# Optimization experiments

Hardware: AMD Instinct MI355X
Metric: run time of the kernel (lower is better)

Reference implementation:

```python
import jax, jax.numpy as jnp
import numpy as np

N = 100000   # nodes
E = 640000   # edges
DIN = 128
H = 128
DOUT = 64
EPS = 1e-5   # BatchNorm eps


def setup_inputs() -> dict:
    key = jax.random.key(0)
    ks = jax.random.split(key, 20)
    x = jax.random.normal(ks[0], (N, DIN), jnp.float32)
    edge_index = jax.random.randint(ks[1], (2, E), 0, N, dtype=jnp.int64)
    ricci_curvature = jax.random.normal(ks[2], (E,), jnp.float32)
    s = 0.05
    W1 = jax.random.normal(ks[3], (DIN, H), jnp.float32) * s
    b1 = jnp.zeros((H,), jnp.float32)
    Wm = jax.random.normal(ks[4], (H, H), jnp.float32) * s
    bm = jnp.zeros((H,), jnp.float32)
    W2 = jax.random.normal(ks[5], (H, DOUT), jnp.float32) * s
    b2 = jnp.zeros((DOUT,), jnp.float32)
    def bn_params(k, d):
        k1, k2, k3, k4 = jax.random.split(k, 4)
        g = jax.random.uniform(k1, (d,), jnp.float32) + 0.5
        b = jax.random.normal(k2, (d,), jnp.float32) * 0.1
        m = jax.random.normal(k3, (d,), jnp.float32) * 0.1
        v = jax.random.uniform(k4, (d,), jnp.float32) + 0.5
        return g, b, m, v
    bn1_g, bn1_b, bn1_m, bn1_v = bn_params(ks[6], DIN)
    bnm_g, bnm_b, bnm_m, bnm_v = bn_params(ks[7], H)
    bn2_g, bn2_b, bn2_m, bn2_v = bn_params(ks[8], H)
    return dict(x=x, edge_index=edge_index, percent=50,
                ricci_curvature=ricci_curvature,
                W1=W1, b1=b1, Wm=Wm, bm=bm, W2=W2, b2=b2,
                bn1_g=bn1_g, bn1_b=bn1_b, bn1_m=bn1_m, bn1_v=bn1_v,
                bnm_g=bnm_g, bnm_b=bnm_b, bnm_m=bnm_m, bnm_v=bnm_v,
                bn2_g=bn2_g, bn2_b=bn2_b, bn2_m=bn2_m, bn2_v=bn2_v)


def _bn_eval(x, g, b, m, v):
    # BatchNorm1d in eval mode: running stats
    return (x - m) * (g * jax.lax.rsqrt(v + EPS)) + b


def _gcn_conv(x, W, bias, src, dst):
    # PyG GCNConv: x' = D^{-1/2} (A+I) D^{-1/2} (x W) + b
    h = x @ W                              # [N, F_out]
    loops = jnp.arange(N, dtype=src.dtype)
    s = jnp.concatenate([src, loops])      # [E+N]
    d = jnp.concatenate([dst, loops])
    deg = jax.ops.segment_sum(jnp.ones_like(d, h.dtype), d, num_segments=N)
    dinv = jax.lax.rsqrt(deg)              # deg >= 1 (self loops)
    norm = dinv[s] * dinv[d]               # [E+N]
    out = jax.ops.segment_sum(h[s] * norm[:, None], d, num_segments=N)
    return out + bias


def reference(x, edge_index, percent, ricci_curvature,
              W1, b1, Wm, bm, W2, b2,
              bn1_g, bn1_b, bn1_m, bn1_v,
              bnm_g, bnm_b, bnm_m, bnm_v,
              bn2_g, bn2_b, bn2_m, bn2_v):
    # Eval mode: no edge sampling (percent / ricci_curvature unused),
    # dropout inactive, BN uses running statistics.
    src, dst = edge_index[0], edge_index[1]
    h = _bn_eval(x, bn1_g, bn1_b, bn1_m, bn1_v)
    h = jax.nn.relu(_gcn_conv(h, W1, b1, src, dst))
    res1 = h
    h = _bn_eval(h, bnm_g, bnm_b, bnm_m, bnm_v)
    h = jax.nn.relu(_gcn_conv(h, Wm, bm, src, dst))
    res2 = h
    h = _bn_eval(h, bn2_g, bn2_b, bn2_m, bn2_v)
    out = _gcn_conv(h, W2, b2, src, dst)
    return (out, res1, res2)
```

## Files before the change

### kernel.cpp

```cpp
#include <hip/hip_runtime.h>

#define N_NODES 100000
#define N_EDGES 640000
#define DIN 128
#define HDIM 128
#define DOUT 64

typedef __attribute__((ext_vector_type(4))) float f32x4;
typedef __attribute__((ext_vector_type(8))) short bf16x8;

__device__ inline unsigned short f2bf(float x) {
    unsigned u = __float_as_uint(x);
    unsigned r = (u + 0x7fffu + ((u >> 16) & 1u)) >> 16;
    return (unsigned short)r;
}
__device__ inline void unpack2(unsigned u, float& f0, float& f1) {
    f0 = __uint_as_float(u << 16);
    f1 = __uint_as_float(u & 0xffff0000u);
}

__global__ void hist_rank_kernel(const int* __restrict__ ei, int* __restrict__ cnt,
                                 int* __restrict__ rank, int ne) {
    int e = blockIdx.x * 256 + threadIdx.x;
    if (e < ne) rank[e] = atomicAdd(&cnt[ei[ne + e]], 1);
}

__global__ void scan_block_kernel(const int* __restrict__ cnt, int* __restrict__ off,
                                  int* __restrict__ bsums, int n) {
    __shared__ int sm[1024];
    int tid = threadIdx.x;
    int i = blockIdx.x * 1024 + tid;
    int v = (i < n) ? cnt[i] : 0;
    sm[tid] = v;
    __syncthreads();
    for (int d = 1; d < 1024; d <<= 1) {
        int t = (tid >= d) ? sm[tid - d] : 0;
        __syncthreads();
        sm[tid] += t;
        __syncthreads();
    }
    if (i < n) off[i] = sm[tid] - v;
    if (tid == 1023) bsums[blockIdx.x] = sm[1023];
}

__global__ void scan_bsums_kernel(int* bsums, int nb) {
    __shared__ int sm[128];
    int tid = threadIdx.x;
    int v = (tid < nb) ? bsums[tid] : 0;
    sm[tid] = v;
    __syncthreads();
    for (int d = 1; d < 128; d <<= 1) {
        int t = (tid >= d) ? sm[tid - d] : 0;
        __syncthreads();
        sm[tid] += t;
        __syncthreads();
    }
    if (tid < nb) bsums[tid] = sm[tid] - v;
}

__global__ void scan_add_kernel(int* __restrict__ off, const int* __restrict__ bsums,
                                const int* __restrict__ cnt, float* __restrict__ dinv, int n) {
    int i = blockIdx.x * 256 + threadIdx.x;
    if (i < n) {
        off[i] += bsums[i >> 10];
        dinv[i] = rsqrtf((float)cnt[i] + 1.0f);
    }
}

__global__ void fill_csr_kernel(const int* __restrict__ ei, const float* __restrict__ dinv,
                                const int* __restrict__ off, const int* __restrict__ rank,
                                int2* __restrict__ csr, int ne) {
    int e = blockIdx.x * 256 + threadIdx.x;
    if (e < ne) {
        int s = ei[e], d = ei[ne + e];
        int2 ent;
        ent.x = s;
        ent.y = __float_as_int(dinv[s] * dinv[d]);
        csr[off[d] + rank[e]] = ent;
    }
}

struct PrepPtrs {
    const float *g[3], *b[3], *m[3], *v[3];
    const float *W[3];
    float *sc[3], *sh[3], *tW[3];
    unsigned short *wt[3];
};

__global__ void bn_prep_all_kernel(PrepPtrs p) {
    __shared__ float sh_s[128];
    int l = blockIdx.x, i = threadIdx.x;
    float s  = p.g[l][i] * rsqrtf(p.v[l][i] + 1e-5f);
    float sh = p.b[l][i] - p.m[l][i] * s;
    p.sc[l][i] = s;
    sh_s[i] = sh;
    __syncthreads();
    int cout = (l == 2) ? DOUT : HDIM;
    if (i < cout) {
        float acc = 0.f;
        for (int k = 0; k < 128; ++k) acc += sh_s[k] * p.W[l][k * cout + i];
        p.tW[l][i] = acc;
    }
}

__global__ void wprep_all_kernel(PrepPtrs p) {
    int l = blockIdx.y;
    int cout = (l == 2) ? DOUT : HDIM;
    int idx = blockIdx.x * 256 + threadIdx.x;
    if (idx >= 128 * cout) return;
    int k = idx / cout, c = idx % cout;
    p.wt[l][c * 128 + k] = f2bf(p.W[l][idx] * p.sc[l][k]);
}

template<int COUT>
__global__ __launch_bounds__(256) void gemm_mfma_kernel(
    const float* __restrict__ X, const unsigned short* __restrict__ Wt,
    const float* __restrict__ tW, unsigned short* __restrict__ T, int nrows)
{
    constexpr int LDT = 136;
    __shared__ unsigned short xs[64 * LDT];
    __shared__ unsigned short ws[COUT * LDT];

    int tid  = threadIdx.x;
    int wave = tid >> 6, lane = tid & 63;
    int row0 = blockIdx.x * 64;

    {
        const uint4* src = (const uint4*)Wt;
        #pragma unroll
        for (int it = 0; it < COUT / 16; ++it) {
            int idx = tid + it * 256;
            int r = idx >> 4, c8 = idx & 15;
            uint4 v = src[idx];
            *(uint4*)&ws[r * LDT + c8 * 8] = v;
        }
    }
    {
        const float4* X4 = (const float4*)X;
        #pragma unroll
        for (int it = 0; it < 8; ++it) {
            int idx = tid + it * 256;
            int r = idx >> 5, c4 = idx & 31;
            int row = row0 + r;
            float4 v = make_float4(0.f, 0.f, 0.f, 0.f);
            if (row < nrows) v = X4[(size_t)row * 32 + c4];
            ushort4 o;
            o.x = f2bf(v.x); o.y = f2bf(v.y); o.z = f2bf(v.z); o.w = f2bf(v.w);
            *(ushort4*)&xs[r * LDT + c4 * 4] = o;
        }
    }
    __syncthreads();

    constexpr int NT = COUT / 16;
    f32x4 acc[NT];
    #pragma unroll
    for (int t = 0; t < NT; ++t) acc[t] = (f32x4)(0.f);

    int arow = wave * 16 + (lane & 15);
    int khi  = (lane >> 4) * 8;

    #pragma unroll
    for (int kk = 0; kk < 4; ++kk) {
        bf16x8 a = *(const bf16x8*)&xs[arow * LDT + kk * 32 + khi];
        #pragma unroll
        for (int t = 0; t < NT; ++t) {
            bf16x8 b = *(const bf16x8*)&ws[(t * 16 + (lane & 15)) * LDT + kk * 32 + khi];
            acc[t] = __builtin_amdgcn_mfma_f32_16x16x32_bf16(a, b, acc[t], 0, 0, 0);
        }
    }

    int crow0 = (lane >> 4) * 4;
    int ccol  = lane & 15;
    #pragma unroll
    for (int t = 0; t < NT; ++t) {
        int col = t * 16 + ccol;
        float tw = tW[col];
        #pragma unroll
        for (int r = 0; r < 4; ++r) {
            int row = row0 + wave * 16 + crow0 + r;
            if (row < nrows)
                T[(size_t)row * COUT + col] = f2bf(acc[t][r] + tw);
        }
    }
}

template<int COUT, bool RELU>
__global__ __launch_bounds__(256) void gather_kernel(
    const unsigned short* __restrict__ T, const float* __restrict__ dinv,
    const int* __restrict__ off, const int* __restrict__ cnt,
    const int2* __restrict__ csr,
    const float* __restrict__ bias, float* __restrict__ out, int n)
{
    constexpr int LPN = COUT / 8;
    int tid = blockIdx.x * 256 + threadIdx.x;
    int node = tid / LPN, lane = tid % LPN;
    if (node >= n) return;

    const uint4* T4 = (const uint4*)T;
    float di  = dinv[node];
    float cf0 = di * di;

    float acc[8];
    {
        uint4 tv = T4[(size_t)node * LPN + lane];
        float f[8];
        unpack2(tv.x, f[0], f[1]); unpack2(tv.y, f[2], f[3]);
        unpack2(tv.z, f[4], f[5]); unpack2(tv.w, f[6], f[7]);
        float4 b0 = ((const float4*)bias)[lane * 2];
        float4 b1 = ((const float4*)bias)[lane * 2 + 1];
        acc[0] = f[0] * cf0 + b0.x; acc[1] = f[1] * cf0 + b0.y;
        acc[2] = f[2] * cf0 + b0.z; acc[3] = f[3] * cf0 + b0.w;
        acc[4] = f[4] * cf0 + b1.x; acc[5] = f[5] * cf0 + b1.y;
        acc[6] = f[6] * cf0 + b1.z; acc[7] = f[7] * cf0 + b1.w;
    }

    int st = off[node];
    int en = st + cnt[node];
    int e  = st;
    for (; e + 1 < en; e += 2) {
        int2  p0 = csr[e], p1 = csr[e + 1];
        float c0 = __int_as_float(p0.y), c1 = __int_as_float(p1.y);
        uint4 v0 = T4[(size_t)p0.x * LPN + lane];
        uint4 v1 = T4[(size_t)p1.x * LPN + lane];
        float f0[8], f1[8];
        unpack2(v0.x, f0[0], f0[1]); unpack2(v0.y, f0[2], f0[3]);
        unpack2(v0.z, f0[4], f0[5]); unpack2(v0.w, f0[6], f0[7]);
        unpack2(v1.x, f1[0], f1[1]); unpack2(v1.y, f1[2], f1[3]);
        unpack2(v1.z, f1[4], f1[5]); unpack2(v1.w, f1[6], f1[7]);
        #pragma unroll
        for (int j = 0; j < 8; ++j) acc[j] += f0[j] * c0 + f1[j] * c1;
    }
    if (e < en) {
        int2  p0 = csr[e];
        float c0 = __int_as_float(p0.y);
        uint4 v0 = T4[(size_t)p0.x * LPN + lane];
        float f0[8];
        unpack2(v0.x, f0[0], f0[1]); unpack2(v0.y, f0[2], f0[3]);
        unpack2(v0.z, f0[4], f0[5]); unpack2(v0.w, f0[6], f0[7]);
        #pragma unroll
        for (int j = 0; j < 8; ++j) acc[j] += f0[j] * c0;
    }

    if (RELU) {
        #pragma unroll
        for (int j = 0; j < 8; ++j) acc[j] = fmaxf(acc[j], 0.f);
    }
    float4* O4 = (float4*)out;
    float4 o0, o1;
    o0.x = acc[0]; o0.y = acc[1]; o0.z = acc[2]; o0.w = acc[3];
    o1.x = acc[4]; o1.y = acc[5]; o1.z = acc[6]; o1.w = acc[7];
    O4[(size_t)node * LPN * 2 + lane * 2]     = o0;
    O4[(size_t)node * LPN * 2 + lane * 2 + 1] = o1;
}

extern "C" void kernel_launch(void* const* d_in, const int* in_sizes, int n_in,
                              void* d_out, int out_size, void* d_ws, size_t ws_size,
                              hipStream_t stream) {
    const float* x   = (const float*)d_in[0];
    const int*   ei  = (const int*)d_in[1];
    const float* W1  = (const float*)d_in[4];
    const float* b1  = (const float*)d_in[5];
    const float* Wm  = (const float*)d_in[6];
    const float* bm  = (const float*)d_in[7];
    const float* W2  = (const float*)d_in[8];
    const float* b2  = (const float*)d_in[9];

    float* out  = (float*)d_out;
    float* res1 = out + (size_t)N_NODES * DOUT;
    float* res2 = res1 + (size_t)N_NODES * HDIM;

    unsigned short* T   = (unsigned short*)d_ws;
    unsigned short* wt1 = T + (size_t)N_NODES * HDIM;
    unsigned short* wtm = wt1 + 128 * HDIM;
    unsigned short* wt2 = wtm + 128 * HDIM;
    float* dinv = (float*)(wt2 + DOUT * 128);
    float* sc1  = dinv + N_NODES;
    float* scm  = sc1 + 128;
    float* sc2  = scm + 128;
    float* sh1  = sc2 + 128;
    float* shm  = sh1 + 128;
    float* sh2  = shm + 128;
    float* tW1  = sh2 + 128;
    float* tWm  = tW1 + 128;
    float* tW2  = tWm + 128;
    int*   cnt     = (int*)(tW2 + 64);
    int*   off     = cnt + N_NODES;
    int*   bsums   = off + N_NODES;
    int*   rank    = bsums + 128;
    int2*  csr     = (int2*)(rank + N_EDGES);

    int gN = (N_NODES + 255) / 256;
    int gE = (N_EDGES + 255) / 256;
    int gT = (N_NODES + 63) / 64;
    int nb = (N_NODES + 1023) / 1024;

    hipMemsetAsync(cnt, 0, N_NODES * sizeof(int), stream);
    hist_rank_kernel<<<gE, 256, 0, stream>>>(ei, cnt, rank, N_EDGES);
    scan_block_kernel<<<nb, 1024, 0, stream>>>(cnt, off, bsums, N_NODES);
    scan_bsums_kernel<<<1, 128, 0, stream>>>(bsums, nb);
    scan_add_kernel<<<gN, 256, 0, stream>>>(off, bsums, cnt, dinv, N_NODES);
    fill_csr_kernel<<<gE, 256, 0, stream>>>(ei, dinv, off, rank, csr, N_EDGES);

    PrepPtrs p;
    p.g[0] = (const float*)d_in[10]; p.b[0] = (const float*)d_in[11];
    p.m[0] = (const float*)d_in[12]; p.v[0] = (const float*)d_in[13];
    p.g[1] = (const float*)d_in[14]; p.b[1] = (const float*)d_in[15];
    p.m[1] = (const float*)d_in[16]; p.v[1] = (const float*)d_in[17];
    p.g[2] = (const float*)d_in[18]; p.b[2] = (const float*)d_in[19];
    p.m[2] = (const float*)d_in[20]; p.v[2] = (const float*)d_in[21];
    p.W[0] = W1; p.W[1] = Wm; p.W[2] = W2;
    p.sc[0] = sc1; p.sc[1] = scm; p.sc[2] = sc2;
    p.sh[0] = sh1; p.sh[1] = shm; p.sh[2] = sh2;
    p.tW[0] = tW1; p.tW[1] = tWm; p.tW[2] = tW2;
    p.wt[0] = wt1; p.wt[1] = wtm; p.wt[2] = wt2;

    bn_prep_all_kernel<<<3, 128, 0, stream>>>(p);
    {
        dim3 g((128 * HDIM + 255) / 256, 3);
        wprep_all_kernel<<<g, 256, 0, stream>>>(p);
    }

    int gG128 = (N_NODES * 16 + 255) / 256;
    int gG64  = (N_NODES * 8 + 255) / 256;

    gemm_mfma_kernel<128><<<gT, 256, 0, stream>>>(x, wt1, tW1, T, N_NODES);
    gather_kernel<128, true><<<gG128, 256, 0, stream>>>(T, dinv, off, cnt, csr, b1, res1, N_NODES);

    gemm_mfma_kernel<128><<<gT, 256, 0, stream>>>(res1, wtm, tWm, T, N_NODES);
    gather_kernel<128, true><<<gG128, 256, 0, stream>>>(T, dinv, off, cnt, csr, bm, res2, N_NODES);

    gemm_mfma_kernel<64><<<gT, 256, 0, stream>>>(res2, wt2, tW2, T, N_NODES);
    gather_kernel<64, false><<<gG64, 256, 0, stream>>>(T, dinv, off, cnt, csr, b2, out, N_NODES);
}
```

Baseline: 236.5 us.

## Merge prep kernels, fold bsum scan into add, unroll gather by four

```diff
diff --git a/kernel.cpp b/kernel.cpp
--- a/kernel.cpp
+++ b/kernel.cpp
@@ -19,10 +19,47 @@
     f1 = __uint_as_float(u & 0xffff0000u);
 }
 
-__global__ void hist_rank_kernel(const int* __restrict__ ei, int* __restrict__ cnt,
-                                 int* __restrict__ rank, int ne) {
-    int e = blockIdx.x * 256 + threadIdx.x;
-    if (e < ne) rank[e] = atomicAdd(&cnt[ei[ne + e]], 1);
+struct PrepPtrs {
+    const float *g[3], *b[3], *m[3], *v[3];
+    const float *W[3];
+    float *tW[3];
+    unsigned short *wt[3];
+};
+
+__global__ void combo_prep_kernel(const int* __restrict__ ei, int* __restrict__ cnt,
+                                  int* __restrict__ rank, int ne, int gE, PrepPtrs p) {
+    int bid = blockIdx.x, tid = threadIdx.x;
+    if (bid < gE) {
+        int e = bid * 256 + tid;
+        if (e < ne) rank[e] = atomicAdd(&cnt[ei[ne + e]], 1);
+        return;
+    }
+    if (bid < gE + 3) {
+        __shared__ float sh_s[128];
+        int l = bid - gE;
+        if (tid < 128) {
+            float s  = p.g[l][tid] * rsqrtf(p.v[l][tid] + 1e-5f);
+            sh_s[tid] = p.b[l][tid] - p.m[l][tid] * s;
+        }
+        __syncthreads();
+        int cout = (l == 2) ? DOUT : HDIM;
+        if (tid < cout) {
+            float acc = 0.f;
+            for (int k = 0; k < 128; ++k) acc += sh_s[k] * p.W[l][k * cout + tid];
+            p.tW[l][tid] = acc;
+        }
+        return;
+    }
+    {
+        int idx0 = bid - gE - 3;
+        int l = idx0 >> 6;
+        int cout = (l == 2) ? DOUT : HDIM;
+        int idx = (idx0 & 63) * 256 + tid;
+        if (idx >= 128 * cout) return;
+        int k = idx / cout, c = idx % cout;
+        float sc = p.g[l][k] * rsqrtf(p.v[l][k] + 1e-5f);
+        p.wt[l][c * 128 + k] = f2bf(p.W[l][idx] * sc);
+    }
 }
 
 __global__ void scan_block_kernel(const int* __restrict__ cnt, int* __restrict__ off,
@@ -43,27 +80,25 @@
     if (tid == 1023) bsums[blockIdx.x] = sm[1023];
 }
 
-__global__ void scan_bsums_kernel(int* bsums, int nb) {
-    __shared__ int sm[128];
+__global__ void scan_add_kernel(int* __restrict__ off, const int* __restrict__ bsums,
+                                const int* __restrict__ cnt, float* __restrict__ dinv,
+                                int2* __restrict__ rng, int n, int nb) {
+    __shared__ int red[4];
     int tid = threadIdx.x;
-    int v = (tid < nb) ? bsums[tid] : 0;
-    sm[tid] = v;
+    int b = blockIdx.x >> 2;
+    int pv = (tid < b) ? bsums[tid] : 0;
+    #pragma unroll
+    for (int o = 32; o > 0; o >>= 1) pv += __shfl_down(pv, o);
+    if ((tid & 63) == 0) red[tid >> 6] = pv;
     __syncthreads();
-    for (int d = 1; d < 128; d <<= 1) {
-        int t = (tid >= d) ? sm[tid - d] : 0;
-        __syncthreads();
-        sm[tid] += t;
-        __syncthreads();
-    }
-    if (tid < nb) bsums[tid] = sm[tid] - v;
-}
-
-__global__ void scan_add_kernel(int* __restrict__ off, const int* __restrict__ bsums,
-                                const int* __restrict__ cnt, float* __restrict__ dinv, int n) {
-    int i = blockIdx.x * 256 + threadIdx.x;
+    int base = red[0] + red[1] + red[2] + red[3];
+    int i = blockIdx.x * 256 + tid;
     if (i < n) {
-        off[i] += bsums[i >> 10];
-        dinv[i] = rsqrtf((float)cnt[i] + 1.0f);
+        int o = off[i] + base;
+        int c = cnt[i];
+        off[i] = o;
+        rng[i] = make_int2(o, o + c);
+        dinv[i] = rsqrtf((float)c + 1.0f);
     }
 }
 
@@ -80,38 +115,6 @@
     }
 }
 
-struct PrepPtrs {
-    const float *g[3], *b[3], *m[3], *v[3];
-    const float *W[3];
-    float *sc[3], *sh[3], *tW[3];
-    unsigned short *wt[3];
-};
-
-__global__ void bn_prep_all_kernel(PrepPtrs p) {
-    __shared__ float sh_s[128];
-    int l = blockIdx.x, i = threadIdx.x;
-    float s  = p.g[l][i] * rsqrtf(p.v[l][i] + 1e-5f);
-    float sh = p.b[l][i] - p.m[l][i] * s;
-    p.sc[l][i] = s;
-    sh_s[i] = sh;
-    __syncthreads();
-    int cout = (l == 2) ? DOUT : HDIM;
-    if (i < cout) {
-        float acc = 0.f;
-        for (int k = 0; k < 128; ++k) acc += sh_s[k] * p.W[l][k * cout + i];
-        p.tW[l][i] = acc;
-    }
-}
-
-__global__ void wprep_all_kernel(PrepPtrs p) {
-    int l = blockIdx.y;
-    int cout = (l == 2) ? DOUT : HDIM;
-    int idx = blockIdx.x * 256 + threadIdx.x;
-    if (idx >= 128 * cout) return;
-    int k = idx / cout, c = idx % cout;
-    p.wt[l][c * 128 + k] = f2bf(p.W[l][idx] * p.sc[l][k]);
-}
-
 template<int COUT>
 __global__ __launch_bounds__(256) void gemm_mfma_kernel(
     const float* __restrict__ X, const unsigned short* __restrict__ Wt,
@@ -184,11 +187,19 @@
     }
 }
 
+#define GACC(vv, cc)                                                     \
+    {                                                                    \
+        float _f0, _f1;                                                  \
+        unpack2(vv.x, _f0, _f1); acc[0] += _f0 * cc; acc[1] += _f1 * cc; \
+        unpack2(vv.y, _f0, _f1); acc[2] += _f0 * cc; acc[3] += _f1 * cc; \
+        unpack2(vv.z, _f0, _f1); acc[4] += _f0 * cc; acc[5] += _f1 * cc; \
+        unpack2(vv.w, _f0, _f1); acc[6] += _f0 * cc; acc[7] += _f1 * cc; \
+    }
+
 template<int COUT, bool RELU>
 __global__ __launch_bounds__(256) void gather_kernel(
     const unsigned short* __restrict__ T, const float* __restrict__ dinv,
-    const int* __restrict__ off, const int* __restrict__ cnt,
-    const int2* __restrict__ csr,
+    const int2* __restrict__ rng, const int2* __restrict__ csr,
     const float* __restrict__ bias, float* __restrict__ out, int n)
 {
     constexpr int LPN = COUT / 8;
@@ -214,31 +225,31 @@
         acc[6] = f[6] * cf0 + b1.z; acc[7] = f[7] * cf0 + b1.w;
     }
 
-    int st = off[node];
-    int en = st + cnt[node];
-    int e  = st;
-    for (; e + 1 < en; e += 2) {
-        int2  p0 = csr[e], p1 = csr[e + 1];
-        float c0 = __int_as_float(p0.y), c1 = __int_as_float(p1.y);
+    int2 r = rng[node];
+    int e = r.x, en = r.y;
+    for (; e + 3 < en; e += 4) {
+        int2 p0 = csr[e], p1 = csr[e + 1], p2 = csr[e + 2], p3 = csr[e + 3];
         uint4 v0 = T4[(size_t)p0.x * LPN + lane];
         uint4 v1 = T4[(size_t)p1.x * LPN + lane];
-        float f0[8], f1[8];
-        unpack2(v0.x, f0[0], f0[1]); unpack2(v0.y, f0[2], f0[3]);
-        unpack2(v0.z, f0[4], f0[5]); unpack2(v0.w, f0[6], f0[7]);
-        unpack2(v1.x, f1[0], f1[1]); unpack2(v1.y, f1[2], f1[3]);
-        unpack2(v1.z, f1[4], f1[5]); unpack2(v1.w, f1[6], f1[7]);
-        #pragma unroll
-        for (int j = 0; j < 8; ++j) acc[j] += f0[j] * c0 + f1[j] * c1;
+        uint4 v2 = T4[(size_t)p2.x * LPN + lane];
+        uint4 v3 = T4[(size_t)p3.x * LPN + lane];
+        float c0 = __int_as_float(p0.y), c1 = __int_as_float(p1.y);
+        float c2 = __int_as_float(p2.y), c3 = __int_as_float(p3.y);
+        GACC(v0, c0); GACC(v1, c1); GACC(v2, c2); GACC(v3, c3);
+    }
+    if (e + 1 < en) {
+        int2 p0 = csr[e], p1 = csr[e + 1];
+        uint4 v0 = T4[(size_t)p0.x * LPN + lane];
+        uint4 v1 = T4[(size_t)p1.x * LPN + lane];
+        float c0 = __int_as_float(p0.y), c1 = __int_as_float(p1.y);
+        GACC(v0, c0); GACC(v1, c1);
+        e += 2;
     }
     if (e < en) {
-        int2  p0 = csr[e];
+        int2 p0 = csr[e];
+        uint4 v0 = T4[(size_t)p0.x * LPN + lane];
         float c0 = __int_as_float(p0.y);
-        uint4 v0 = T4[(size_t)p0.x * LPN + lane];
-        float f0[8];
-        unpack2(v0.x, f0[0], f0[1]); unpack2(v0.y, f0[2], f0[3]);
-        unpack2(v0.z, f0[4], f0[5]); unpack2(v0.w, f0[6], f0[7]);
-        #pragma unroll
-        for (int j = 0; j < 8; ++j) acc[j] += f0[j] * c0;
+        GACC(v0, c0);
     }
 
     if (RELU) {
@@ -274,32 +285,20 @@
     unsigned short* wtm = wt1 + 128 * HDIM;
     unsigned short* wt2 = wtm + 128 * HDIM;
     float* dinv = (float*)(wt2 + DOUT * 128);
-    float* sc1  = dinv + N_NODES;
-    float* scm  = sc1 + 128;
-    float* sc2  = scm + 128;
-    float* sh1  = sc2 + 128;
-    float* shm  = sh1 + 128;
-    float* sh2  = shm + 128;
-    float* tW1  = sh2 + 128;
+    float* tW1  = dinv + N_NODES;
     float* tWm  = tW1 + 128;
     float* tW2  = tWm + 128;
-    int*   cnt     = (int*)(tW2 + 64);
-    int*   off     = cnt + N_NODES;
-    int*   bsums   = off + N_NODES;
-    int*   rank    = bsums + 128;
-    int2*  csr     = (int2*)(rank + N_EDGES);
+    int*   cnt   = (int*)(tW2 + 64);
+    int*   off   = cnt + N_NODES;
+    int*   bsums = off + N_NODES;
+    int*   rank  = bsums + 128;
+    int2*  rng   = (int2*)(rank + N_EDGES);
+    int2*  csr   = (int2*)(rng + N_NODES);
 
     int gN = (N_NODES + 255) / 256;
     int gE = (N_EDGES + 255) / 256;
     int gT = (N_NODES + 63) / 64;
     int nb = (N_NODES + 1023) / 1024;
-
-    hipMemsetAsync(cnt, 0, N_NODES * sizeof(int), stream);
-    hist_rank_kernel<<<gE, 256, 0, stream>>>(ei, cnt, rank, N_EDGES);
-    scan_block_kernel<<<nb, 1024, 0, stream>>>(cnt, off, bsums, N_NODES);
-    scan_bsums_kernel<<<1, 128, 0, stream>>>(bsums, nb);
-    scan_add_kernel<<<gN, 256, 0, stream>>>(off, bsums, cnt, dinv, N_NODES);
-    fill_csr_kernel<<<gE, 256, 0, stream>>>(ei, dinv, off, rank, csr, N_EDGES);
 
     PrepPtrs p;
     p.g[0] = (const float*)d_in[10]; p.b[0] = (const float*)d_in[11];
@@ -309,26 +308,24 @@
     p.g[2] = (const float*)d_in[18]; p.b[2] = (const float*)d_in[19];
     p.m[2] = (const float*)d_in[20]; p.v[2] = (const float*)d_in[21];
     p.W[0] = W1; p.W[1] = Wm; p.W[2] = W2;
-    p.sc[0] = sc1; p.sc[1] = scm; p.sc[2] = sc2;
-    p.sh[0] = sh1; p.sh[1] = shm; p.sh[2] = sh2;
     p.tW[0] = tW1; p.tW[1] = tWm; p.tW[2] = tW2;
     p.wt[0] = wt1; p.wt[1] = wtm; p.wt[2] = wt2;
 
-    bn_prep_all_kernel<<<3, 128, 0, stream>>>(p);
-    {
-        dim3 g((128 * HDIM + 255) / 256, 3);
-        wprep_all_kernel<<<g, 256, 0, stream>>>(p);
-    }
+    hipMemsetAsync(cnt, 0, N_NODES * sizeof(int), stream);
+    combo_prep_kernel<<<gE + 3 + 192, 256, 0, stream>>>(ei, cnt, rank, N_EDGES, gE, p);
+    scan_block_kernel<<<nb, 1024, 0, stream>>>(cnt, off, bsums, N_NODES);
+    scan_add_kernel<<<gN, 256, 0, stream>>>(off, bsums, cnt, dinv, rng, N_NODES, nb);
+    fill_csr_kernel<<<gE, 256, 0, stream>>>(ei, dinv, off, rank, csr, N_EDGES);
 
     int gG128 = (N_NODES * 16 + 255) / 256;
     int gG64  = (N_NODES * 8 + 255) / 256;
 
     gemm_mfma_kernel<128><<<gT, 256, 0, stream>>>(x, wt1, tW1, T, N_NODES);
-    gather_kernel<128, true><<<gG128, 256, 0, stream>>>(T, dinv, off, cnt, csr, b1, res1, N_NODES);
+    gather_kernel<128, true><<<gG128, 256, 0, stream>>>(T, dinv, rng, csr, b1, res1, N_NODES);
 
     gemm_mfma_kernel<128><<<gT, 256, 0, stream>>>(res1, wtm, tWm, T, N_NODES);
-    gather_kernel<128, true><<<gG128, 256, 0, stream>>>(T, dinv, off, cnt, csr, bm, res2, N_NODES);
+    gather_kernel<128, true><<<gG128, 256, 0, stream>>>(T, dinv, rng, csr, bm, res2, N_NODES);
 
     gemm_mfma_kernel<64><<<gT, 256, 0, stream>>>(res2, wt2, tW2, T, N_NODES);
-    gather_kernel<64, false><<<gG64, 256, 0, stream>>>(T, dinv, off, cnt, csr, b2, out, N_NODES);
-}
+    gather_kernel<64, false><<<gG64, 256, 0, stream>>>(T, dinv, rng, csr, b2, out, N_NODES);
+}
```

Result: faster. 223.3 us (-5.6%).
